# Optimization experiments

Measured on AMD Instinct MI355X. Metric: run time of the kernel, lower is better.

## Reference

```python
import jax, jax.numpy as jnp
import numpy as np


def setup_inputs() -> dict:
    key = jax.random.key(0)
    ks = jax.random.split(key, 9)
    B, C, H, W = 16, 64, 64, 64
    s = 0.02
    return {
        "x": jax.random.normal(ks[0], (B, C, H, W), dtype=jnp.float32),
        "qw": jax.random.normal(ks[1], (C, C), dtype=jnp.float32) * s,
        "qb": jax.random.normal(ks[2], (C,), dtype=jnp.float32) * s,
        "kw": jax.random.normal(ks[3], (C, C), dtype=jnp.float32) * s,
        "kb": jax.random.normal(ks[4], (C,), dtype=jnp.float32) * s,
        "vw": jax.random.normal(ks[5], (C, C), dtype=jnp.float32) * s,
        "vb": jax.random.normal(ks[6], (C,), dtype=jnp.float32) * s,
        "ow": jax.random.normal(ks[7], (C, C), dtype=jnp.float32) * s,
        "ob": jax.random.normal(ks[8], (C,), dtype=jnp.float32) * s,
    }


def reference(x, qw, qb, kw, kb, vw, vb, ow, ob):
    # x: [B, C, H, W]; 1x1 convs == per-pixel linear maps with weight [out_ch, in_ch]
    B, C, H, W = x.shape
    S = H * W
    xt = x.reshape(B, C, S).transpose(0, 2, 1)  # [B, S, C] tokens over spatial positions
    Q = jnp.einsum("bsc,oc->bso", xt, qw) + qb
    K = jnp.einsum("bsc,oc->bso", xt, kw) + kb
    V = jnp.einsum("bsc,oc->bso", xt, vw) + vb
    scale = 1.0 / jnp.sqrt(jnp.asarray(C, dtype=x.dtype))
    scores = jnp.einsum("bqc,bkc->bqk", Q, K) * scale  # [B, S, S]
    attn = jax.nn.softmax(scores, axis=-1)
    out = jnp.einsum("bqk,bkc->bqc", attn, V)  # [B, S, C]
    out = jnp.einsum("bsc,oc->bso", out, ow) + ob  # out 1x1 conv
    return out.transpose(0, 2, 1).reshape(B, C, H, W)
```

## Files before the change

kernel.cpp:

```cpp
#include <hip/hip_runtime.h>
#include <stdint.h>

#define SS 4096
#define CC 64
#define BB 16

typedef unsigned short u16;
typedef __attribute__((ext_vector_type(8))) __bf16 bf16x8;
typedef __attribute__((ext_vector_type(8))) short short8;
typedef __attribute__((ext_vector_type(4))) short s16x4;
typedef __attribute__((ext_vector_type(4))) float f32x4;

__device__ __forceinline__ uint32_t pkbf(float a, float b) {
    uint32_t ua = __float_as_uint(a) + 0x8000u;
    uint32_t ub = __float_as_uint(b) + 0x8000u;
    return __builtin_amdgcn_perm(ub, ua, 0x07060302u);
}

__device__ __forceinline__ bf16x8 ldw8(const float* p) {
    f32x4 lo = *(const f32x4*)(p);
    f32x4 hi = *(const f32x4*)(p + 4);
    union { uint32_t u[4]; bf16x8 v; } r;
    r.u[0] = pkbf(lo[0], lo[1]);
    r.u[1] = pkbf(lo[2], lo[3]);
    r.u[2] = pkbf(hi[0], hi[1]);
    r.u[3] = pkbf(hi[2], hi[3]);
    return r.v;
}

__global__ __launch_bounds__(256, 4) void qkv_kernel(
    const float* __restrict__ x,
    const float* __restrict__ qw, const float* __restrict__ qb,
    const float* __restrict__ kw, const float* __restrict__ kb,
    const float* __restrict__ vw, const float* __restrict__ vb,
    u16* __restrict__ Q, u16* __restrict__ K, u16* __restrict__ VT)
{
    const int b    = blockIdx.x & 15;
    const int s0   = (blockIdx.x >> 4) << 6;
    const int tid  = threadIdx.x;
    const int w    = tid >> 6;
    const int lane = tid & 63;
    const int lq   = lane & 15;
    const int quad = lane >> 4;

    __shared__ u16 wt[3][64 * 72];
    __shared__ u16 xt[64 * 72];

    for (int m = 0; m < 3; ++m) {
        const float* wsrc = (m == 0) ? qw : ((m == 1) ? kw : vw);
#pragma unroll
        for (int i = 0; i < 8; ++i) {
            int p  = tid + (i << 8);
            int o  = p >> 5;
            int cp = p & 31;
            const float* wp = wsrc + o * 64 + cp * 2;
            ((uint32_t*)&wt[m][o * 72])[cp] = pkbf(wp[0], wp[1]);
        }
    }
    {
        const int sl = tid & 63;
        const int g  = tid >> 6;
        const float* xp = x + (size_t)b * CC * SS + s0 + sl;
#pragma unroll
        for (int i = 0; i < 8; ++i) {
            int p = g + (i << 2);
            float f0 = xp[(size_t)(2 * p) * SS];
            float f1 = xp[(size_t)(2 * p + 1) * SS];
            ((uint32_t*)&xt[sl * 72])[p] = pkbf(f0, f1);
        }
    }
    __syncthreads();

    bf16x8 a0 = *(const bf16x8*)&xt[(w * 16 + lq) * 72 + quad * 8];
    bf16x8 a1 = *(const bf16x8*)&xt[(w * 16 + lq) * 72 + 32 + quad * 8];
    __syncthreads();

    u16* bb = xt + w * (16 * 72);

    const float QSCALE = 0.125f * 1.44269504088896340736f;

    for (int m = 0; m < 3; ++m) {
        const float* bsrc = (m == 0) ? qb : ((m == 1) ? kb : vb);
        bf16x8 bfr[2][4];
#pragma unroll
        for (int kc = 0; kc < 2; ++kc)
#pragma unroll
            for (int nt = 0; nt < 4; ++nt)
                bfr[kc][nt] = *(const bf16x8*)&wt[m][(nt * 16 + lq) * 72 + kc * 32 + quad * 8];

        f32x4 acc[4];
#pragma unroll
        for (int nt = 0; nt < 4; ++nt) {
            float bv = bsrc[nt * 16 + lq];
            acc[nt] = (f32x4){bv, bv, bv, bv};
        }
#pragma unroll
        for (int nt = 0; nt < 4; ++nt) {
            acc[nt] = __builtin_amdgcn_mfma_f32_16x16x32_bf16(a0, bfr[0][nt], acc[nt], 0, 0, 0);
            acc[nt] = __builtin_amdgcn_mfma_f32_16x16x32_bf16(a1, bfr[1][nt], acc[nt], 0, 0, 0);
        }

        if (m == 2) {
#pragma unroll
            for (int nt = 0; nt < 4; ++nt) {
                int c = nt * 16 + lq;
                uint2 pv;
                pv.x = pkbf(acc[nt][0], acc[nt][1]);
                pv.y = pkbf(acc[nt][2], acc[nt][3]);
                *(uint2*)(VT + ((size_t)(b * CC + c)) * SS + s0 + w * 16 + quad * 4) = pv;
            }
        } else {
            const float scl = (m == 0) ? QSCALE : 1.0f;
#pragma unroll
            for (int nt = 0; nt < 4; ++nt)
#pragma unroll
                for (int r = 0; r < 4; ++r)
                    bb[(quad * 4 + r) * 72 + nt * 16 + lq] =
                        (u16)((__float_as_uint(acc[nt][r] * scl) + 0x8000u) >> 16);

            const int row = lane >> 2;
            const int ch  = (lane & 3) << 4;
            short8 v0 = *(const short8*)&bb[row * 72 + ch];
            short8 v1 = *(const short8*)&bb[row * 72 + ch + 8];
            u16* dst = ((m == 0) ? Q : K) + ((size_t)(b * SS + s0 + w * 16 + row)) * CC + ch;
            *(short8*)dst = v0;
            *(short8*)(dst + 8) = v1;
        }
    }
}

__global__ __launch_bounds__(256, 2) void flash_kernel(
    const u16* __restrict__ Q, const u16* __restrict__ K,
    const u16* __restrict__ Vt, const float* __restrict__ ow,
    const float* __restrict__ ob, float* __restrict__ out)
{
    const int b    = blockIdx.x & 15;
    const int q0   = (blockIdx.x >> 4) << 7;
    const int tid  = threadIdx.x;
    const int w    = tid >> 6;
    const int lane = tid & 63;
    const int lq   = lane & 15;
    const int quad = lane >> 4;

    __shared__ u16 lds_k[2][64 * 64];
    __shared__ u16 lds_v[2][64 * 64];
    __shared__ u16 lds_p[8][16 * 64];

    bf16x8 qf[2][2];
#pragma unroll
    for (int g = 0; g < 2; ++g) {
        const u16* qp = Q + ((size_t)(b * SS + q0 + g * 64 + w * 16 + lq)) * CC + quad * 8;
        qf[g][0] = *(const bf16x8*)(qp);
        qf[g][1] = *(const bf16x8*)(qp + 32);
    }

    f32x4 ot[2][4];
#pragma unroll
    for (int g = 0; g < 2; ++g)
#pragma unroll
        for (int ct = 0; ct < 4; ++ct) ot[g][ct] = (f32x4){0.f, 0.f, 0.f, 0.f};
    float lp[2][4] = {{0.f, 0.f, 0.f, 0.f}, {0.f, 0.f, 0.f, 0.f}};

    const int srow = tid >> 2;
    const int a    = tid & 3;
    const u16* kg = K + ((size_t)(b * SS + srow)) * CC + a * 16;
    const u16* vg = Vt + ((size_t)(b * CC + srow)) * SS + a * 16;
    const int ssw = srow & 7;
    const int sw0 = srow * 64 + ((((a << 1)    ) ^ ssw) << 3);
    const int sw1 = srow * 64 + ((((a << 1) | 1) ^ ssw) << 3);
    const int kcs = (a >> 1) << 2;
    const int us  = (a & 1) << 2;
    const int vw0 = srow * 64 + (((kcs + 0) ^ ssw) << 3) + us;
    const int vw1 = srow * 64 + (((kcs + 1) ^ ssw) << 3) + us;
    const int vw2 = srow * 64 + (((kcs + 2) ^ ssw) << 3) + us;
    const int vw3 = srow * 64 + (((kcs + 3) ^ ssw) << 3) + us;

    {
        short8 k0 = *(const short8*)(kg);
        short8 k1 = *(const short8*)(kg + 8);
        union { short8 v; s16x4 h[2]; } v0, v1;
        v0.v = *(const short8*)(vg);
        v1.v = *(const short8*)(vg + 8);
        *(short8*)&lds_k[0][sw0] = k0;
        *(short8*)&lds_k[0][sw1] = k1;
        *(s16x4*)&lds_v[0][vw0] = v0.h[0];
        *(s16x4*)&lds_v[0][vw1] = v0.h[1];
        *(s16x4*)&lds_v[0][vw2] = v1.h[0];
        *(s16x4*)&lds_v[0][vw3] = v1.h[1];
    }

    const int lsw = lq & 7;
    u16* pw0 = lds_p[(w << 1)];
    u16* pw1 = lds_p[(w << 1) | 1];

    for (int kt = 0; kt < 64; ++kt) {
        __syncthreads();
        const int buf = kt & 1;

        const int ktn = (kt + 1) & 63;
        const u16* kgn = kg + (size_t)ktn * (64 * CC);
        const u16* vgn = vg + ktn * 64;
        short8 nk0 = *(const short8*)(kgn);
        short8 nk1 = *(const short8*)(kgn + 8);
        union { short8 v; s16x4 h[2]; } nv0, nv1;
        nv0.v = *(const short8*)(vgn);
        nv1.v = *(const short8*)(vgn + 8);

        bf16x8 kf[2][4];
#pragma unroll
        for (int kc = 0; kc < 2; ++kc)
#pragma unroll
            for (int mt = 0; mt < 4; ++mt)
                kf[kc][mt] = *(const bf16x8*)
                    &lds_k[buf][(mt * 16 + lq) * 64 + (((kc << 2) + quad) ^ lsw) * 8];

        f32x4 sa[2][4];
#pragma unroll
        for (int g = 0; g < 2; ++g)
#pragma unroll
            for (int mt = 0; mt < 4; ++mt) sa[g][mt] = (f32x4){0.f, 0.f, 0.f, 0.f};
        __builtin_amdgcn_s_setprio(1);
#pragma unroll
        for (int g = 0; g < 2; ++g)
#pragma unroll
            for (int kc = 0; kc < 2; ++kc)
#pragma unroll
                for (int mt = 0; mt < 4; ++mt)
                    sa[g][mt] = __builtin_amdgcn_mfma_f32_16x16x32_bf16(
                        kf[kc][mt], qf[g][kc], sa[g][mt], 0, 0, 0);
        __builtin_amdgcn_s_setprio(0);

        bf16x8 vf[2][4];
#pragma unroll
        for (int kc = 0; kc < 2; ++kc)
#pragma unroll
            for (int ct = 0; ct < 4; ++ct)
                vf[kc][ct] = *(const bf16x8*)
                    &lds_v[buf][(ct * 16 + lq) * 64 + (((kc << 2) + quad) ^ lsw) * 8];

#pragma unroll
        for (int g = 0; g < 2; ++g) {
            union { uint32_t u[4]; bf16x8 v; } pf[2];
#pragma unroll
            for (int mt = 0; mt < 4; ++mt) {
                float p0 = __builtin_amdgcn_exp2f(sa[g][mt][0]);
                float p1 = __builtin_amdgcn_exp2f(sa[g][mt][1]);
                float p2 = __builtin_amdgcn_exp2f(sa[g][mt][2]);
                float p3 = __builtin_amdgcn_exp2f(sa[g][mt][3]);
                lp[g][0] += p0; lp[g][1] += p1; lp[g][2] += p2; lp[g][3] += p3;
                pf[mt >> 1].u[(mt & 1) * 2 + 0] = pkbf(p0, p1);
                pf[mt >> 1].u[(mt & 1) * 2 + 1] = pkbf(p2, p3);
            }
            __builtin_amdgcn_s_setprio(1);
#pragma unroll
            for (int kc = 0; kc < 2; ++kc)
#pragma unroll
                for (int ct = 0; ct < 4; ++ct)
                    ot[g][ct] = __builtin_amdgcn_mfma_f32_16x16x32_bf16(
                        vf[kc][ct], pf[kc].v, ot[g][ct], 0, 0, 0);
            __builtin_amdgcn_s_setprio(0);
        }

        u16* lkd = lds_k[buf ^ 1];
        u16* lvd = lds_v[buf ^ 1];
        *(short8*)&lkd[sw0] = nk0;
        *(short8*)&lkd[sw1] = nk1;
        *(s16x4*)&lvd[vw0] = nv0.h[0];
        *(s16x4*)&lvd[vw1] = nv0.h[1];
        *(s16x4*)&lvd[vw2] = nv1.h[0];
        *(s16x4*)&lvd[vw3] = nv1.h[1];
    }

    bf16x8 wf[2][4];
#pragma unroll
    for (int kc = 0; kc < 2; ++kc)
#pragma unroll
        for (int nt = 0; nt < 4; ++nt)
            wf[kc][nt] = ldw8(ow + (nt * 16 + lq) * 64 + kc * 32 + quad * 8);
    float bias[4];
#pragma unroll
    for (int nt = 0; nt < 4; ++nt) bias[nt] = ob[nt * 16 + lq];

#pragma unroll
    for (int g = 0; g < 2; ++g) {
        float l = (lp[g][0] + lp[g][1]) + (lp[g][2] + lp[g][3]);
        l += __shfl_xor(l, 16);
        l += __shfl_xor(l, 32);
        const float inv = 1.0f / l;

        u16* po = g ? pw1 : pw0;
#pragma unroll
        for (int ct = 0; ct < 4; ++ct) {
            uint2 pv;
            pv.x = pkbf(ot[g][ct][0] * inv, ot[g][ct][1] * inv);
            pv.y = pkbf(ot[g][ct][2] * inv, ot[g][ct][3] * inv);
            *(uint2*)&po[lq * 64 + (((ct * 2 + (quad >> 1)) ^ lsw) << 3) + (quad & 1) * 4] = pv;
        }
        bf16x8 oa0 = *(const bf16x8*)&po[lq * 64 + (((0 * 4 + quad) ^ lsw) << 3)];
        bf16x8 oa1 = *(const bf16x8*)&po[lq * 64 + (((1 * 4 + quad) ^ lsw) << 3)];

        f32x4 acc[4];
#pragma unroll
        for (int nt = 0; nt < 4; ++nt)
            acc[nt] = (f32x4){bias[nt], bias[nt], bias[nt], bias[nt]};
#pragma unroll
        for (int nt = 0; nt < 4; ++nt) {
            acc[nt] = __builtin_amdgcn_mfma_f32_16x16x32_bf16(oa0, wf[0][nt], acc[nt], 0, 0, 0);
            acc[nt] = __builtin_amdgcn_mfma_f32_16x16x32_bf16(oa1, wf[1][nt], acc[nt], 0, 0, 0);
        }
#pragma unroll
        for (int nt = 0; nt < 4; ++nt) {
            float* dst = out + ((size_t)(b * CC + nt * 16 + lq)) * SS
                       + q0 + g * 64 + w * 16 + quad * 4;
            *(f32x4*)dst = acc[nt];
        }
    }
}

extern "C" void kernel_launch(void* const* d_in, const int* in_sizes, int n_in,
                              void* d_out, int out_size, void* d_ws, size_t ws_size,
                              hipStream_t stream)
{
    const float* x  = (const float*)d_in[0];
    const float* qw = (const float*)d_in[1];
    const float* qb = (const float*)d_in[2];
    const float* kw = (const float*)d_in[3];
    const float* kb = (const float*)d_in[4];
    const float* vw = (const float*)d_in[5];
    const float* vb = (const float*)d_in[6];
    const float* ow = (const float*)d_in[7];
    const float* ob = (const float*)d_in[8];
    float* out = (float*)d_out;

    const size_t T = (size_t)BB * SS * CC;
    u16* Q  = (u16*)d_ws;
    u16* K  = Q + T;
    u16* VT = K + T;

    qkv_kernel<<<dim3(BB * 64), dim3(256), 0, stream>>>(x, qw, qb, kw, kb, vw, vb, Q, K, VT);
    flash_kernel<<<dim3(BB * 32), dim3(256), 0, stream>>>(Q, K, VT, ow, ob, out);
}
```

Baseline: 168.8 us.

## Load V fragments directly from global memory instead of staging through LDS

Removes the double-buffered LDS staging for the transposed V tile: each lane now reads its V MFMA fragment as two 8-byte global loads per tile, taken straight from Vt with the k-permutation that matches the register layout. This drops the LDS writes and reads for V and halves LDS use, which may raise occupancy. The cost is uncoalesced, latency-exposed global loads issued inside the loop with no prefetch, leaving the PV MFMAs to wait on L2/HBM. It also seeds the first QK MFMA with a zero accumulator instead of zero-initialising the accumulators first.

```diff
diff --git a/kernel.cpp b/kernel.cpp
--- a/kernel.cpp
+++ b/kernel.cpp
@@ -143,7 +143,6 @@
     const int quad = lane >> 4;
 
     __shared__ u16 lds_k[2][64 * 64];
-    __shared__ u16 lds_v[2][64 * 64];
     __shared__ u16 lds_p[8][16 * 64];
 
     bf16x8 qf[2][2];
@@ -161,32 +160,28 @@
         for (int ct = 0; ct < 4; ++ct) ot[g][ct] = (f32x4){0.f, 0.f, 0.f, 0.f};
     float lp[2][4] = {{0.f, 0.f, 0.f, 0.f}, {0.f, 0.f, 0.f, 0.f}};
 
+    const f32x4 ZV = (f32x4){0.f, 0.f, 0.f, 0.f};
+
     const int srow = tid >> 2;
     const int a    = tid & 3;
     const u16* kg = K + ((size_t)(b * SS + srow)) * CC + a * 16;
-    const u16* vg = Vt + ((size_t)(b * CC + srow)) * SS + a * 16;
     const int ssw = srow & 7;
     const int sw0 = srow * 64 + ((((a << 1)    ) ^ ssw) << 3);
     const int sw1 = srow * 64 + ((((a << 1) | 1) ^ ssw) << 3);
-    const int kcs = (a >> 1) << 2;
-    const int us  = (a & 1) << 2;
-    const int vw0 = srow * 64 + (((kcs + 0) ^ ssw) << 3) + us;
-    const int vw1 = srow * 64 + (((kcs + 1) ^ ssw) << 3) + us;
-    const int vw2 = srow * 64 + (((kcs + 2) ^ ssw) << 3) + us;
-    const int vw3 = srow * 64 + (((kcs + 3) ^ ssw) << 3) + us;
+
+    const u16* vbase[2][4];
+#pragma unroll
+    for (int kc = 0; kc < 2; ++kc)
+#pragma unroll
+        for (int ct = 0; ct < 4; ++ct)
+            vbase[kc][ct] = Vt + ((size_t)(b * CC + ct * 16 + lq)) * SS
+                          + kc * 32 + quad * 4;
 
     {
         short8 k0 = *(const short8*)(kg);
         short8 k1 = *(const short8*)(kg + 8);
-        union { short8 v; s16x4 h[2]; } v0, v1;
-        v0.v = *(const short8*)(vg);
-        v1.v = *(const short8*)(vg + 8);
         *(short8*)&lds_k[0][sw0] = k0;
         *(short8*)&lds_k[0][sw1] = k1;
-        *(s16x4*)&lds_v[0][vw0] = v0.h[0];
-        *(s16x4*)&lds_v[0][vw1] = v0.h[1];
-        *(s16x4*)&lds_v[0][vw2] = v1.h[0];
-        *(s16x4*)&lds_v[0][vw3] = v1.h[1];
     }
 
     const int lsw = lq & 7;
@@ -196,15 +191,12 @@
     for (int kt = 0; kt < 64; ++kt) {
         __syncthreads();
         const int buf = kt & 1;
+        const int kb  = kt << 6;
 
         const int ktn = (kt + 1) & 63;
         const u16* kgn = kg + (size_t)ktn * (64 * CC);
-        const u16* vgn = vg + ktn * 64;
         short8 nk0 = *(const short8*)(kgn);
         short8 nk1 = *(const short8*)(kgn + 8);
-        union { short8 v; s16x4 h[2]; } nv0, nv1;
-        nv0.v = *(const short8*)(vgn);
-        nv1.v = *(const short8*)(vgn + 8);
 
         bf16x8 kf[2][4];
 #pragma unroll
@@ -215,28 +207,29 @@
                     &lds_k[buf][(mt * 16 + lq) * 64 + (((kc << 2) + quad) ^ lsw) * 8];
 
         f32x4 sa[2][4];
+        __builtin_amdgcn_s_setprio(1);
 #pragma unroll
         for (int g = 0; g < 2; ++g)
 #pragma unroll
-            for (int mt = 0; mt < 4; ++mt) sa[g][mt] = (f32x4){0.f, 0.f, 0.f, 0.f};
-        __builtin_amdgcn_s_setprio(1);
-#pragma unroll
-        for (int g = 0; g < 2; ++g)
-#pragma unroll
-            for (int kc = 0; kc < 2; ++kc)
-#pragma unroll
-                for (int mt = 0; mt < 4; ++mt)
-                    sa[g][mt] = __builtin_amdgcn_mfma_f32_16x16x32_bf16(
-                        kf[kc][mt], qf[g][kc], sa[g][mt], 0, 0, 0);
+            for (int mt = 0; mt < 4; ++mt) {
+                sa[g][mt] = __builtin_amdgcn_mfma_f32_16x16x32_bf16(
+                    kf[0][mt], qf[g][0], ZV, 0, 0, 0);
+                sa[g][mt] = __builtin_amdgcn_mfma_f32_16x16x32_bf16(
+                    kf[1][mt], qf[g][1], sa[g][mt], 0, 0, 0);
+            }
         __builtin_amdgcn_s_setprio(0);
 
         bf16x8 vf[2][4];
 #pragma unroll
         for (int kc = 0; kc < 2; ++kc)
 #pragma unroll
-            for (int ct = 0; ct < 4; ++ct)
-                vf[kc][ct] = *(const bf16x8*)
-                    &lds_v[buf][(ct * 16 + lq) * 64 + (((kc << 2) + quad) ^ lsw) * 8];
+            for (int ct = 0; ct < 4; ++ct) {
+                const u16* vp = vbase[kc][ct] + kb;
+                union { s16x4 h[2]; bf16x8 v; } vv;
+                vv.h[0] = *(const s16x4*)(vp);
+                vv.h[1] = *(const s16x4*)(vp + 16);
+                vf[kc][ct] = vv.v;
+            }
 
 #pragma unroll
         for (int g = 0; g < 2; ++g) {
@@ -262,13 +255,8 @@
         }
 
         u16* lkd = lds_k[buf ^ 1];
-        u16* lvd = lds_v[buf ^ 1];
         *(short8*)&lkd[sw0] = nk0;
         *(short8*)&lkd[sw1] = nk1;
-        *(s16x4*)&lvd[vw0] = nv0.h[0];
-        *(s16x4*)&lvd[vw1] = nv0.h[1];
-        *(s16x4*)&lvd[vw2] = nv1.h[0];
-        *(s16x4*)&lvd[vw3] = nv1.h[1];
     }
 
     bf16x8 wf[2][4];
```

Result: slower. 328.9 us (+94.9%).

## Split key tile across wave pairs with cross-wave output reduction in flash kernel

Applied to the files above, without the earlier changes.

Restructures the flash attention loop so each pair of waves shares 64 queries and splits the 64-key tile in halves. Each wave now does 4 query tiles against 2 key subtiles, and the partial O accumulators and row sums are reduced through shared memory at the end. This cuts per-wave K/V LDS fragment loads (K 8→4, V 8→4 per iteration) at the cost of more accumulator registers and an extra reduction step. It also swaps the manual bf16 pack for the hardware v_cvt_pk_bf16_f32 instruction for the probability values.

```diff
diff --git a/kernel.cpp b/kernel.cpp
--- a/kernel.cpp
+++ b/kernel.cpp
@@ -15,6 +15,12 @@
     uint32_t ua = __float_as_uint(a) + 0x8000u;
     uint32_t ub = __float_as_uint(b) + 0x8000u;
     return __builtin_amdgcn_perm(ub, ua, 0x07060302u);
+}
+
+__device__ __forceinline__ uint32_t cvtpk(float a, float b) {
+    uint32_t r;
+    asm("v_cvt_pk_bf16_f32 %0, %1, %2" : "=v"(r) : "v"(a), "v"(b));
+    return r;
 }
 
 __device__ __forceinline__ bf16x8 ldw8(const float* p) {
@@ -141,25 +147,36 @@
     const int lane = tid & 63;
     const int lq   = lane & 15;
     const int quad = lane >> 4;
-
-    __shared__ u16 lds_k[2][64 * 64];
-    __shared__ u16 lds_v[2][64 * 64];
-    __shared__ u16 lds_p[8][16 * 64];
-
-    bf16x8 qf[2][2];
-#pragma unroll
-    for (int g = 0; g < 2; ++g) {
-        const u16* qp = Q + ((size_t)(b * SS + q0 + g * 64 + w * 16 + lq)) * CC + quad * 8;
-        qf[g][0] = *(const bf16x8*)(qp);
-        qf[g][1] = *(const bf16x8*)(qp + 32);
-    }
-
-    f32x4 ot[2][4];
-#pragma unroll
-    for (int g = 0; g < 2; ++g)
-#pragma unroll
-        for (int ct = 0; ct < 4; ++ct) ot[g][ct] = (f32x4){0.f, 0.f, 0.f, 0.f};
-    float lp[2][4] = {{0.f, 0.f, 0.f, 0.f}, {0.f, 0.f, 0.f, 0.f}};
+    const int wk   = w & 1;
+    const int wq   = w >> 1;
+
+    __shared__ u16 smem[4 * 4096];
+    __shared__ u16 lds_p[8][1024];
+    __shared__ float lpbuf[8][16];
+
+    u16* lds_k = smem;
+    u16* lds_v = smem + 2 * 4096;
+
+    bf16x8 qf[4][2];
+#pragma unroll
+    for (int qt = 0; qt < 4; ++qt) {
+        const u16* qp = Q + ((size_t)(b * SS + q0 + wq * 64 + qt * 16 + lq)) * CC + quad * 8;
+        qf[qt][0] = *(const bf16x8*)(qp);
+        qf[qt][1] = *(const bf16x8*)(qp + 32);
+    }
+
+    f32x4 ot[4][4];
+#pragma unroll
+    for (int qt = 0; qt < 4; ++qt)
+#pragma unroll
+        for (int ct = 0; ct < 4; ++ct) ot[qt][ct] = (f32x4){0.f, 0.f, 0.f, 0.f};
+    float lp[4][4];
+#pragma unroll
+    for (int qt = 0; qt < 4; ++qt)
+#pragma unroll
+        for (int r = 0; r < 4; ++r) lp[qt][r] = 0.f;
+
+    const f32x4 ZV = (f32x4){0.f, 0.f, 0.f, 0.f};
 
     const int srow = tid >> 2;
     const int a    = tid & 3;
@@ -181,21 +198,21 @@
         union { short8 v; s16x4 h[2]; } v0, v1;
         v0.v = *(const short8*)(vg);
         v1.v = *(const short8*)(vg + 8);
-        *(short8*)&lds_k[0][sw0] = k0;
-        *(short8*)&lds_k[0][sw1] = k1;
-        *(s16x4*)&lds_v[0][vw0] = v0.h[0];
-        *(s16x4*)&lds_v[0][vw1] = v0.h[1];
-        *(s16x4*)&lds_v[0][vw2] = v1.h[0];
-        *(s16x4*)&lds_v[0][vw3] = v1.h[1];
+        *(short8*)&lds_k[sw0] = k0;
+        *(short8*)&lds_k[sw1] = k1;
+        *(s16x4*)&lds_v[vw0] = v0.h[0];
+        *(s16x4*)&lds_v[vw1] = v0.h[1];
+        *(s16x4*)&lds_v[vw2] = v1.h[0];
+        *(s16x4*)&lds_v[vw3] = v1.h[1];
     }
 
     const int lsw = lq & 7;
-    u16* pw0 = lds_p[(w << 1)];
-    u16* pw1 = lds_p[(w << 1) | 1];
 
     for (int kt = 0; kt < 64; ++kt) {
         __syncthreads();
         const int buf = kt & 1;
+        u16* lkb = lds_k + buf * 4096;
+        u16* lvb = lds_v + buf * 4096;
 
         const int ktn = (kt + 1) & 63;
         const u16* kgn = kg + (size_t)ktn * (64 * CC);
@@ -206,63 +223,59 @@
         nv0.v = *(const short8*)(vgn);
         nv1.v = *(const short8*)(vgn + 8);
 
-        bf16x8 kf[2][4];
+        bf16x8 kf[2][2];
 #pragma unroll
         for (int kc = 0; kc < 2; ++kc)
 #pragma unroll
-            for (int mt = 0; mt < 4; ++mt)
+            for (int mt = 0; mt < 2; ++mt)
                 kf[kc][mt] = *(const bf16x8*)
-                    &lds_k[buf][(mt * 16 + lq) * 64 + (((kc << 2) + quad) ^ lsw) * 8];
-
-        f32x4 sa[2][4];
-#pragma unroll
-        for (int g = 0; g < 2; ++g)
-#pragma unroll
-            for (int mt = 0; mt < 4; ++mt) sa[g][mt] = (f32x4){0.f, 0.f, 0.f, 0.f};
-        __builtin_amdgcn_s_setprio(1);
-#pragma unroll
-        for (int g = 0; g < 2; ++g)
-#pragma unroll
-            for (int kc = 0; kc < 2; ++kc)
-#pragma unroll
-                for (int mt = 0; mt < 4; ++mt)
-                    sa[g][mt] = __builtin_amdgcn_mfma_f32_16x16x32_bf16(
-                        kf[kc][mt], qf[g][kc], sa[g][mt], 0, 0, 0);
-        __builtin_amdgcn_s_setprio(0);
-
-        bf16x8 vf[2][4];
-#pragma unroll
-        for (int kc = 0; kc < 2; ++kc)
+                    &lkb[((wk * 2 + mt) * 16 + lq) * 64 + (((kc << 2) + quad) ^ lsw) * 8];
+
+        bf16x8 vf[4];
+#pragma unroll
+        for (int ct = 0; ct < 4; ++ct)
+            vf[ct] = *(const bf16x8*)
+                &lvb[(ct * 16 + lq) * 64 + (((wk << 2) + quad) ^ lsw) * 8];
+
+#pragma unroll
+        for (int qt = 0; qt < 4; ++qt) {
+            f32x4 s0, s1;
+            __builtin_amdgcn_s_setprio(1);
+            s0 = __builtin_amdgcn_mfma_f32_16x16x32_bf16(kf[0][0], qf[qt][0], ZV, 0, 0, 0);
+            s0 = __builtin_amdgcn_mfma_f32_16x16x32_bf16(kf[1][0], qf[qt][1], s0, 0, 0, 0);
+            s1 = __builtin_amdgcn_mfma_f32_16x16x32_bf16(kf[0][1], qf[qt][0], ZV, 0, 0, 0);
+            s1 = __builtin_amdgcn_mfma_f32_16x16x32_bf16(kf[1][1], qf[qt][1], s1, 0, 0, 0);
+            __builtin_amdgcn_s_setprio(0);
+
+            float p00 = __builtin_amdgcn_exp2f(s0[0]);
+            float p01 = __builtin_amdgcn_exp2f(s0[1]);
+            float p02 = __builtin_amdgcn_exp2f(s0[2]);
+            float p03 = __builtin_amdgcn_exp2f(s0[3]);
+            float p10 = __builtin_amdgcn_exp2f(s1[0]);
+            float p11 = __builtin_amdgcn_exp2f(s1[1]);
+            float p12 = __builtin_amdgcn_exp2f(s1[2]);
+            float p13 = __builtin_amdgcn_exp2f(s1[3]);
+            lp[qt][0] += p00 + p10;
+            lp[qt][1] += p01 + p11;
+            lp[qt][2] += p02 + p12;
+            lp[qt][3] += p03 + p13;
+
+            union { uint32_t u[4]; bf16x8 v; } pf;
+            pf.u[0] = cvtpk(p00, p01);
+            pf.u[1] = cvtpk(p02, p03);
+            pf.u[2] = cvtpk(p10, p11);
+            pf.u[3] = cvtpk(p12, p13);
+
+            __builtin_amdgcn_s_setprio(1);
 #pragma unroll
             for (int ct = 0; ct < 4; ++ct)
-                vf[kc][ct] = *(const bf16x8*)
-                    &lds_v[buf][(ct * 16 + lq) * 64 + (((kc << 2) + quad) ^ lsw) * 8];
-
-#pragma unroll
-        for (int g = 0; g < 2; ++g) {
-            union { uint32_t u[4]; bf16x8 v; } pf[2];
-#pragma unroll
-            for (int mt = 0; mt < 4; ++mt) {
-                float p0 = __builtin_amdgcn_exp2f(sa[g][mt][0]);
-                float p1 = __builtin_amdgcn_exp2f(sa[g][mt][1]);
-                float p2 = __builtin_amdgcn_exp2f(sa[g][mt][2]);
-                float p3 = __builtin_amdgcn_exp2f(sa[g][mt][3]);
-                lp[g][0] += p0; lp[g][1] += p1; lp[g][2] += p2; lp[g][3] += p3;
-                pf[mt >> 1].u[(mt & 1) * 2 + 0] = pkbf(p0, p1);
-                pf[mt >> 1].u[(mt & 1) * 2 + 1] = pkbf(p2, p3);
-            }
-            __builtin_amdgcn_s_setprio(1);
-#pragma unroll
-            for (int kc = 0; kc < 2; ++kc)
-#pragma unroll
-                for (int ct = 0; ct < 4; ++ct)
-                    ot[g][ct] = __builtin_amdgcn_mfma_f32_16x16x32_bf16(
-                        vf[kc][ct], pf[kc].v, ot[g][ct], 0, 0, 0);
+                ot[qt][ct] = __builtin_amdgcn_mfma_f32_16x16x32_bf16(
+                    vf[ct], pf.v, ot[qt][ct], 0, 0, 0);
             __builtin_amdgcn_s_setprio(0);
         }
 
-        u16* lkd = lds_k[buf ^ 1];
-        u16* lvd = lds_v[buf ^ 1];
+        u16* lkd = lds_k + (buf ^ 1) * 4096;
+        u16* lvd = lds_v + (buf ^ 1) * 4096;
         *(short8*)&lkd[sw0] = nk0;
         *(short8*)&lkd[sw1] = nk1;
         *(s16x4*)&lvd[vw0] = nv0.h[0];
@@ -271,6 +284,29 @@
         *(s16x4*)&lvd[vw3] = nv1.h[1];
     }
 
+    __syncthreads();
+
+    float lsum[4];
+#pragma unroll
+    for (int qt = 0; qt < 4; ++qt) {
+        float l = (lp[qt][0] + lp[qt][1]) + (lp[qt][2] + lp[qt][3]);
+        l += __shfl_xor(l, 16);
+        l += __shfl_xor(l, 32);
+        lsum[qt] = l;
+    }
+
+    float* red = (float*)smem;
+    const int oqt0 = (1 - wk) * 2;
+#pragma unroll
+    for (int t = 0; t < 2; ++t) {
+        const int qt = oqt0 + t;
+#pragma unroll
+        for (int ct = 0; ct < 4; ++ct)
+            *(f32x4*)&red[(wq * 4 + qt) * 1024 + lq * 64 + ct * 16 + quad * 4] = ot[qt][ct];
+        lpbuf[wq * 4 + qt][lq] = lsum[qt];
+    }
+    __syncthreads();
+
     bf16x8 wf[2][4];
 #pragma unroll
     for (int kc = 0; kc < 2; ++kc)
@@ -281,19 +317,22 @@
 #pragma unroll
     for (int nt = 0; nt < 4; ++nt) bias[nt] = ob[nt * 16 + lq];
 
-#pragma unroll
-    for (int g = 0; g < 2; ++g) {
-        float l = (lp[g][0] + lp[g][1]) + (lp[g][2] + lp[g][3]);
-        l += __shfl_xor(l, 16);
-        l += __shfl_xor(l, 32);
+    const int kqt0 = wk * 2;
+#pragma unroll
+    for (int t = 0; t < 2; ++t) {
+        const int qt = kqt0 + t;
+#pragma unroll
+        for (int ct = 0; ct < 4; ++ct)
+            ot[qt][ct] += *(const f32x4*)&red[(wq * 4 + qt) * 1024 + lq * 64 + ct * 16 + quad * 4];
+        const float l   = lsum[qt] + lpbuf[wq * 4 + qt][lq];
         const float inv = 1.0f / l;
 
-        u16* po = g ? pw1 : pw0;
+        u16* po = lds_p[wq * 4 + qt];
 #pragma unroll
         for (int ct = 0; ct < 4; ++ct) {
             uint2 pv;
-            pv.x = pkbf(ot[g][ct][0] * inv, ot[g][ct][1] * inv);
-            pv.y = pkbf(ot[g][ct][2] * inv, ot[g][ct][3] * inv);
+            pv.x = pkbf(ot[qt][ct][0] * inv, ot[qt][ct][1] * inv);
+            pv.y = pkbf(ot[qt][ct][2] * inv, ot[qt][ct][3] * inv);
             *(uint2*)&po[lq * 64 + (((ct * 2 + (quad >> 1)) ^ lsw) << 3) + (quad & 1) * 4] = pv;
         }
         bf16x8 oa0 = *(const bf16x8*)&po[lq * 64 + (((0 * 4 + quad) ^ lsw) << 3)];
@@ -311,7 +350,7 @@
 #pragma unroll
         for (int nt = 0; nt < 4; ++nt) {
             float* dst = out + ((size_t)(b * CC + nt * 16 + lq)) * SS
-                       + q0 + g * 64 + w * 16 + quad * 4;
+                       + q0 + wq * 64 + qt * 16 + quad * 4;
             *(f32x4*)dst = acc[nt];
         }
     }
```

Measured after the change: 384.8 us. +128.0%, slower.
